# Kernel optimization log

Hardware: AMD Instinct MI355X
Metric: run time of the kernel (lower is better)

The kernel has to match this reference:

```python
import jax, jax.numpy as jnp
import numpy as np

N_TOKENS = 16384
D_MODEL = 1024
N_EXPERTS = 4
TOP_K = 2
LN_EPS = 1e-6


def setup_inputs() -> dict:
    key = jax.random.key(0)
    ks = jax.random.split(key, 6)
    d, e = D_MODEL, N_EXPERTS
    return {
        "x": jax.random.normal(ks[0], (N_TOKENS, d), jnp.float32),
        "gate_w": jax.random.normal(ks[1], (e, d), jnp.float32) * (1.0 / np.sqrt(d)),
        "w1": jax.random.normal(ks[2], (e, 2 * d, d), jnp.float32) * (1.0 / np.sqrt(d)),
        "b1": jax.random.normal(ks[3], (e, 2 * d), jnp.float32) * 0.01,
        "w2": jax.random.normal(ks[4], (e, d, 2 * d), jnp.float32) * (1.0 / np.sqrt(2 * d)),
        "b2": jax.random.normal(ks[5], (e, d), jnp.float32) * 0.01,
        "gamma": jnp.ones((e, d), jnp.float32),
        "beta": jnp.zeros((e, d), jnp.float32),
    }


def _expert_ffn(x, w1e, b1e, w2e, b2e, ge, be):
    h = jax.nn.gelu(x @ w1e.T + b1e, approximate=False)   # [N, 2d]
    z = x + (h @ w2e.T + b2e)                              # residual, [N, d]
    mu = jnp.mean(z, axis=-1, keepdims=True)
    var = jnp.var(z, axis=-1, keepdims=True)
    return (z - mu) * jax.lax.rsqrt(var + LN_EPS) * ge + be


def reference(x, gate_w, w1, b1, w2, b2, gamma, beta):
    n = x.shape[0]
    scores = x @ gate_w.T                                  # [N, E]
    ew, ei = jax.lax.top_k(scores, TOP_K)                  # [N, K]
    ew = jax.nn.softmax(ew, axis=-1)
    # combine weights: dense [N, E] routing matrix (each row has K nonzeros)
    comb = jnp.zeros_like(scores).at[jnp.arange(n)[:, None], ei].add(ew)
    y = jnp.zeros_like(x)
    for e in range(N_EXPERTS):  # small fixed expert count
        y = y + comb[:, e:e + 1] * _expert_ffn(x, w1[e], b1[e], w2[e], b2[e], gamma[e], beta[e])
    return y
```

## Files before the change

kernel.cpp:

```cpp
#include <hip/hip_runtime.h>
#include <hip/hip_bf16.h>
#include <math.h>

#define NT 16384
#define DM 1024
#define NE 4

typedef __attribute__((ext_vector_type(8))) short short8;
typedef __attribute__((ext_vector_type(4))) float f32x4;

#define GLDS(g, l)                                                        \
  __builtin_amdgcn_global_load_lds(                                       \
      (const __attribute__((address_space(1))) void*)(g),                 \
      (__attribute__((address_space(3))) void*)(l), 16, 0, 0)

__device__ __forceinline__ float bf2f(short h) {
    union { unsigned u; float f; } v;
    v.u = ((unsigned)(unsigned short)h) << 16;
    return v.f;
}

__global__ __launch_bounds__(256) void detect_kernel(
    const unsigned int* __restrict__ xw, int* __restrict__ flag)
{
    __shared__ int red[4];
    const int t = threadIdx.x;
    int cnt = 0;
    #pragma unroll 4
    for (int i = 0; i < 64; ++i) {
        unsigned w = xw[t * 64 + i];
        unsigned e0 = (w >> 7) & 0xFFu;
        cnt += (e0 >= 100u && e0 <= 150u) ? 1 : 0;
    }
    #pragma unroll
    for (int o = 32; o > 0; o >>= 1) cnt += __shfl_xor(cnt, o);
    if ((t & 63) == 0) red[t >> 6] = cnt;
    __syncthreads();
    if (t == 0) {
        int tot = red[0] + red[1] + red[2] + red[3];
        *flag = (tot > 8192) ? 1 : 0;
    }
}

__global__ __launch_bounds__(256) void init_kernel(
    int* __restrict__ counts, int* __restrict__ idx)
{
    const int t = blockIdx.x * 256 + threadIdx.x;
    idx[t] = 0;
    if (t < NE) counts[t] = 0;
}

__global__ __launch_bounds__(256) void convert_big_kernel(
    const float* __restrict__ src, short* __restrict__ dst, int n,
    const int* __restrict__ flag)
{
    if (*flag) return;
    const int stride = gridDim.x * blockDim.x;
    const int t0 = blockIdx.x * blockDim.x + threadIdx.x;
    const float4* s = (const float4*)src;
    for (int i = t0; i < n / 4; i += stride) {
        float4 v = s[i];
        __hip_bfloat16 b0 = __float2bfloat16(v.x);
        __hip_bfloat16 b1 = __float2bfloat16(v.y);
        __hip_bfloat16 b2 = __float2bfloat16(v.z);
        __hip_bfloat16 b3 = __float2bfloat16(v.w);
        short4 o;
        o.x = *(short*)&b0; o.y = *(short*)&b1;
        o.z = *(short*)&b2; o.w = *(short*)&b3;
        *(short4*)(dst + (size_t)i * 4) = o;
    }
}

__global__ __launch_bounds__(256) void convert_small_kernel(
    const void* __restrict__ b1, const void* __restrict__ b2,
    const void* __restrict__ ga, const void* __restrict__ be,
    short* __restrict__ b1d, short* __restrict__ b2d,
    short* __restrict__ gad, short* __restrict__ bed,
    const int* __restrict__ flag)
{
    const int isbf = *flag;
    const int t = blockIdx.x * 256 + threadIdx.x;
    const void* src; short* dst; int i;
    if (t < 8192)      { src = b1; dst = b1d; i = t; }
    else if (t < 12288){ src = b2; dst = b2d; i = t - 8192; }
    else if (t < 16384){ src = ga; dst = gad; i = t - 12288; }
    else               { src = be; dst = bed; i = t - 16384; }
    short v;
    if (isbf) v = ((const short*)src)[i];
    else {
        __hip_bfloat16 b = __float2bfloat16(((const float*)src)[i]);
        v = *(short*)&b;
    }
    dst[i] = v;
}

__global__ __launch_bounds__(256) void gate_kernel(
    const void* __restrict__ x, const void* __restrict__ gw,
    float* __restrict__ comb, int* __restrict__ choice,
    const int* __restrict__ flag)
{
    const int lane  = threadIdx.x & 63;
    const int token = blockIdx.x * 4 + (threadIdx.x >> 6);
    double s0 = 0., s1 = 0., s2 = 0., s3 = 0.;
    if (*flag) {
        const short8* xr = (const short8*)((const short*)x + (size_t)token * DM);
        const short8* g0 = (const short8*)((const short*)gw + 0 * DM);
        const short8* g1 = (const short8*)((const short*)gw + 1 * DM);
        const short8* g2 = (const short8*)((const short*)gw + 2 * DM);
        const short8* g3 = (const short8*)((const short*)gw + 3 * DM);
        #pragma unroll
        for (int c = 0; c < 2; ++c) {
            short8 xv = xr[c * 64 + lane];
            short8 a0 = g0[c * 64 + lane], a1 = g1[c * 64 + lane];
            short8 a2 = g2[c * 64 + lane], a3 = g3[c * 64 + lane];
            #pragma unroll
            for (int j = 0; j < 8; ++j) {
                double xd = (double)bf2f(xv[j]);
                s0 += xd * (double)bf2f(a0[j]);
                s1 += xd * (double)bf2f(a1[j]);
                s2 += xd * (double)bf2f(a2[j]);
                s3 += xd * (double)bf2f(a3[j]);
            }
        }
    } else {
        const float4* xr = (const float4*)((const float*)x + (size_t)token * DM);
        const float4* g0 = (const float4*)((const float*)gw + 0 * DM);
        const float4* g1 = (const float4*)((const float*)gw + 1 * DM);
        const float4* g2 = (const float4*)((const float*)gw + 2 * DM);
        const float4* g3 = (const float4*)((const float*)gw + 3 * DM);
        #pragma unroll
        for (int c = 0; c < 4; ++c) {
            float4 xv = xr[c * 64 + lane];
            float4 a0 = g0[c * 64 + lane], a1 = g1[c * 64 + lane];
            float4 a2 = g2[c * 64 + lane], a3 = g3[c * 64 + lane];
            s0 += (double)xv.x * a0.x + (double)xv.y * a0.y + (double)xv.z * a0.z + (double)xv.w * a0.w;
            s1 += (double)xv.x * a1.x + (double)xv.y * a1.y + (double)xv.z * a1.z + (double)xv.w * a1.w;
            s2 += (double)xv.x * a2.x + (double)xv.y * a2.y + (double)xv.z * a2.z + (double)xv.w * a2.w;
            s3 += (double)xv.x * a3.x + (double)xv.y * a3.y + (double)xv.z * a3.z + (double)xv.w * a3.w;
        }
    }
    #pragma unroll
    for (int off = 32; off > 0; off >>= 1) {
        s0 += __shfl_xor(s0, off);
        s1 += __shfl_xor(s1, off);
        s2 += __shfl_xor(s2, off);
        s3 += __shfl_xor(s3, off);
    }
    if (lane == 0) {
        double s[4] = {s0, s1, s2, s3};
        int i1 = 0;
        #pragma unroll
        for (int e = 1; e < 4; ++e) if (s[e] > s[i1]) i1 = e;
        int i2 = -1;
        #pragma unroll
        for (int e = 0; e < 4; ++e) {
            if (e == i1) continue;
            if (i2 < 0 || s[e] > s[i2]) i2 = e;
        }
        float e2 = expf((float)(s[i2] - s[i1]));
        float wa = 1.0f / (1.0f + e2);
        float wb = e2 * wa;
        float* cr = comb + (size_t)token * 4;
        #pragma unroll
        for (int e = 0; e < 4; ++e)
            cr[e] = (e == i1) ? wa : ((e == i2) ? wb : 0.0f);
        choice[token] = i1 | (i2 << 8);
    }
}

__global__ __launch_bounds__(256) void route_kernel(
    const int* __restrict__ choice, int* __restrict__ counts, int* __restrict__ idx)
{
    __shared__ int T[4][8];
    __shared__ int base[4];
    const int tid = threadIdx.x, w = tid >> 6, lane = tid & 63;
    const int t = blockIdx.x * 256 + tid;
    const int c = choice[t];
    const int e0 = c & 0xFF, e1 = (c >> 8) & 0xFF;
    const unsigned long long lt = ((unsigned long long)1 << lane) - 1;
    int rank0 = 0, rank1 = 0;
    #pragma unroll
    for (int e = 0; e < 4; ++e) {
        unsigned long long m0 = __ballot(e0 == e);
        unsigned long long m1 = __ballot(e1 == e);
        if (e0 == e) rank0 = __popcll(m0 & lt);
        if (e1 == e) rank1 = __popcll(m1 & lt);
        if (lane == 0) { T[w][e] = __popcll(m0); T[w][4 + e] = __popcll(m1); }
    }
    __syncthreads();
    if (tid < 4) {
        int tot = 0;
        #pragma unroll
        for (int w2 = 0; w2 < 4; ++w2) tot += T[w2][tid] + T[w2][4 + tid];
        base[tid] = atomicAdd(&counts[tid], tot);
    }
    __syncthreads();
    int off0 = base[e0], off1 = base[e1];
    #pragma unroll
    for (int w2 = 0; w2 < 4; ++w2) {
        if (w2 < w) off0 += T[w2][e0];
        off1 += T[w2][e1];
        if (w2 < w) off1 += T[w2][4 + e1];
    }
    idx[e0 * NT + off0 + rank0] = t;
    idx[e1 * NT + off1 + rank1] = t;
}

template <int EPI>
__global__ __launch_bounds__(256, 2) void gemm_bt(
    const short* __restrict__ Araw, const short* __restrict__ Acvt,
    const short* __restrict__ Braw, const short* __restrict__ Bcvt,
    const __hip_bfloat16* __restrict__ bias,
    void* __restrict__ Cout,
    const int* __restrict__ idxl,
    const int* __restrict__ count, int c0,
    int N, int K, const int* __restrict__ flag)
{
    const int cnt  = *count - c0;
    const int row0 = blockIdx.y * 128;
    if (row0 >= cnt) return;

    const short* A = (*flag) ? Araw : Acvt;
    const short* B = (*flag) ? Braw : Bcvt;

    __shared__ __align__(16) short sA[128 * 64];
    __shared__ __align__(16) short sB[128 * 64];
    const int tid  = threadIdx.x;
    const int wid  = tid >> 6;
    const int lane = tid & 63;
    const int col0 = blockIdx.x * 128;
    const int wm = wid >> 1, wn = wid & 1;
    const int quad = lane >> 4;
    const int mrow = lane & 15;

    const short* gA[4];
    const short* gB[4];
    #pragma unroll
    for (int r = 0; r < 4; ++r) {
        const int lrow = row0 + wid * 32 + r * 8 + (lane >> 3);
        size_t grow;
        if (EPI == 0) {
            int p = c0 + lrow;
            if (p > NT - 1) p = NT - 1;
            grow = (size_t)idxl[p];
        } else {
            grow = (size_t)lrow;
        }
        gA[r] = A + grow * K + (lane & 7) * 8;
        gB[r] = B + (size_t)(col0 + wid * 32 + r * 8 + (lane >> 3)) * K + (lane & 7) * 8;
    }

    f32x4 acc[4][4];
    #pragma unroll
    for (int i = 0; i < 4; ++i)
        #pragma unroll
        for (int j = 0; j < 4; ++j)
            acc[i][j] = (f32x4){0.f, 0.f, 0.f, 0.f};

    for (int k0 = 0; k0 < K; k0 += 64) {
        #pragma unroll
        for (int r = 0; r < 4; ++r) {
            const int rb = wid * 32 + r * 8;
            GLDS(gA[r] + k0, sA + rb * 64);
            GLDS(gB[r] + k0, sB + rb * 64);
        }
        __syncthreads();
        #pragma unroll
        for (int kk = 0; kk < 64; kk += 32) {
            short8 a[4], b[4];
            #pragma unroll
            for (int t = 0; t < 4; ++t) {
                a[t] = *(const short8*)(sA + (wm * 64 + t * 16 + mrow) * 64 + kk + quad * 8);
                b[t] = *(const short8*)(sB + (wn * 64 + t * 16 + mrow) * 64 + kk + quad * 8);
            }
            #pragma unroll
            for (int mt = 0; mt < 4; ++mt)
                #pragma unroll
                for (int nt = 0; nt < 4; ++nt)
                    acc[mt][nt] = __builtin_amdgcn_mfma_f32_16x16x32_bf16(
                        a[mt], b[nt], acc[mt][nt], 0, 0, 0);
        }
        __syncthreads();
    }

    #pragma unroll
    for (int mt = 0; mt < 4; ++mt) {
        #pragma unroll
        for (int nt = 0; nt < 4; ++nt) {
            const int col = col0 + wn * 64 + nt * 16 + mrow;
            const float bval = __bfloat162float(bias[col]);
            #pragma unroll
            for (int i = 0; i < 4; ++i) {
                const int lrow = row0 + wm * 64 + mt * 16 + quad * 4 + i;
                if (lrow < cnt) {
                    float v = acc[mt][nt][i] + bval;
                    if (EPI == 0) {
                        v = 0.5f * v * (1.0f + erff(v * 0.70710678118654752f));
                        ((__hip_bfloat16*)Cout)[(size_t)lrow * N + col] = __float2bfloat16(v);
                    } else {
                        ((float*)Cout)[(size_t)lrow * N + col] = v;
                    }
                }
            }
        }
    }
}

__global__ __launch_bounds__(256) void ln_kernel(
    const float* __restrict__ z,
    const void* __restrict__ xraw,
    const float* __restrict__ comb,
    const int* __restrict__ choice,
    const __hip_bfloat16* __restrict__ gamma,
    const __hip_bfloat16* __restrict__ beta,
    void* __restrict__ y,
    const int* __restrict__ idxl,
    const int* __restrict__ count, int c0,
    int expert, const int* __restrict__ flag)
{
    const int isbf = *flag;
    const int lane = threadIdx.x & 63;
    const int l    = blockIdx.x * 4 + (threadIdx.x >> 6);
    const int cnt  = *count - c0;
    if (l >= cnt) return;
    const int token = idxl[c0 + l];
    const int ch = choice[token];
    const int e0 = ch & 0xFF, e1 = (ch >> 8) & 0xFF;
    const int firstexp = e0 < e1 ? e0 : e1;
    const int accumulate = (expert != firstexp);

    const f32x4* zr = (const f32x4*)(z + (size_t)l * DM);
    f32x4 v[4];
    float sum = 0.f, ssq = 0.f;
    #pragma unroll
    for (int c = 0; c < 4; ++c) {
        f32x4 zv = zr[c * 64 + lane];
        if (isbf) {
            short4 xv = *(const short4*)((const short*)xraw + (size_t)token * DM + c * 256 + lane * 4);
            v[c][0] = zv[0] + bf2f(xv.x);
            v[c][1] = zv[1] + bf2f(xv.y);
            v[c][2] = zv[2] + bf2f(xv.z);
            v[c][3] = zv[3] + bf2f(xv.w);
        } else {
            float4 xv = *(const float4*)((const float*)xraw + (size_t)token * DM + c * 256 + lane * 4);
            v[c][0] = zv[0] + xv.x;
            v[c][1] = zv[1] + xv.y;
            v[c][2] = zv[2] + xv.z;
            v[c][3] = zv[3] + xv.w;
        }
        #pragma unroll
        for (int j = 0; j < 4; ++j) { sum += v[c][j]; ssq += v[c][j] * v[c][j]; }
    }
    #pragma unroll
    for (int off = 32; off > 0; off >>= 1) {
        sum += __shfl_xor(sum, off);
        ssq += __shfl_xor(ssq, off);
    }
    const float mu   = sum * (1.0f / DM);
    const float var  = fmaxf(ssq * (1.0f / DM) - mu * mu, 0.0f);
    const float rstd = rsqrtf(var + 1e-6f);
    const float w    = comb[(size_t)token * 4 + expert];
    #pragma unroll
    for (int c = 0; c < 4; ++c) {
        #pragma unroll
        for (int j = 0; j < 4; ++j) {
            const int id = c * 256 + lane * 4 + j;
            const float g = __bfloat162float(gamma[id]);
            const float b = __bfloat162float(beta[id]);
            float o = w * ((v[c][j] - mu) * rstd * g + b);
            if (isbf) {
                __hip_bfloat16* yr = (__hip_bfloat16*)y + (size_t)token * DM;
                if (accumulate) o += __bfloat162float(yr[id]);
                yr[id] = __float2bfloat16(o);
            } else {
                float* yr = (float*)y + (size_t)token * DM;
                if (accumulate) o += yr[id];
                yr[id] = o;
            }
        }
    }
}

extern "C" void kernel_launch(void* const* d_in, const int* in_sizes, int n_in,
                              void* d_out, int out_size, void* d_ws, size_t ws_size,
                              hipStream_t stream)
{
    char* ws = (char*)d_ws;
    size_t off = 0;
    auto alloc = [&](size_t bytes) -> char* {
        char* p = ws + off;
        off = (off + bytes + 255) & ~(size_t)255;
        return p;
    };
    int*   flag   = (int*)  alloc(256);
    float* comb   = (float*)alloc((size_t)NT * 4 * sizeof(float));
    int*   choice = (int*)  alloc((size_t)NT * sizeof(int));
    int*   counts = (int*)  alloc(NE * sizeof(int));
    int*   idx    = (int*)  alloc((size_t)NE * NT * sizeof(int));
    short* b1b    = (short*)alloc((size_t)NE * 2 * DM * 2);
    short* b2b    = (short*)alloc((size_t)NE * DM * 2);
    short* gb     = (short*)alloc((size_t)NE * DM * 2);
    short* bb     = (short*)alloc((size_t)NE * DM * 2);
    short* w1b    = (short*)alloc((size_t)NE * 2 * DM * DM * 2);
    short* w2b    = (short*)alloc((size_t)NE * 2 * DM * DM * 2);
    short* xb     = (short*)alloc((size_t)NT * DM * 2);
    const size_t fixed = off;

    int cap = NT;
    while (cap > 512 && fixed + (size_t)cap * 8192 > ws_size) cap >>= 1;
    short* h = (short*)alloc((size_t)cap * 2 * DM * 2);
    float* z = (float*)alloc((size_t)cap * DM * sizeof(float));

    detect_kernel<<<1, 256, 0, stream>>>((const unsigned int*)d_in[0], flag);
    init_kernel<<<(NE * NT) / 256, 256, 0, stream>>>(counts, idx);

    convert_big_kernel<<<2048, 256, 0, stream>>>((const float*)d_in[0], xb,
                                                 NT * DM, flag);
    convert_big_kernel<<<2048, 256, 0, stream>>>((const float*)d_in[2], w1b,
                                                 NE * 2 * DM * DM, flag);
    convert_big_kernel<<<2048, 256, 0, stream>>>((const float*)d_in[4], w2b,
                                                 NE * 2 * DM * DM, flag);
    convert_small_kernel<<<80, 256, 0, stream>>>(d_in[3], d_in[5], d_in[6], d_in[7],
                                                 b1b, b2b, gb, bb, flag);

    gate_kernel<<<NT / 4, 256, 0, stream>>>(d_in[0], d_in[1], comb, choice, flag);
    route_kernel<<<NT / 256, 256, 0, stream>>>(choice, counts, idx);

    for (int e = 0; e < NE; ++e) {
        const short* w1r = (const short*)d_in[2] + (size_t)e * 2 * DM * DM;
        const short* w2r = (const short*)d_in[4] + (size_t)e * 2 * DM * DM;
        const short* w1c = w1b + (size_t)e * 2 * DM * DM;
        const short* w2c = w2b + (size_t)e * 2 * DM * DM;
        const __hip_bfloat16* b1e = (const __hip_bfloat16*)(b1b + (size_t)e * 2 * DM);
        const __hip_bfloat16* b2e = (const __hip_bfloat16*)(b2b + (size_t)e * DM);
        const __hip_bfloat16* ge  = (const __hip_bfloat16*)(gb + (size_t)e * DM);
        const __hip_bfloat16* be  = (const __hip_bfloat16*)(bb + (size_t)e * DM);
        const int* idx_e = idx + (size_t)e * NT;
        const int* cnt_e = counts + e;

        for (int c0 = 0; c0 < NT; c0 += cap) {
            dim3 g1(2 * DM / 128, cap / 128);
            gemm_bt<0><<<g1, 256, 0, stream>>>((const short*)d_in[0], xb,
                                               w1r, w1c, b1e, (void*)h,
                                               idx_e, cnt_e, c0, 2 * DM, DM, flag);

            dim3 g2(DM / 128, cap / 128);
            gemm_bt<1><<<g2, 256, 0, stream>>>(h, h, w2r, w2c, b2e, (void*)z,
                                               idx_e, cnt_e, c0, DM, 2 * DM, flag);

            ln_kernel<<<cap / 4, 256, 0, stream>>>(z, d_in[0], comb, choice, ge, be,
                                                   d_out, idx_e, cnt_e, c0, e, flag);
        }
    }
}
```

Baseline: 891.3 us.

## Batch all experts into single 256x256 double-buffered GEMM launches and fuse LN combine

Replaces the 128x128 single-buffered GEMM with a 256x256-tile, 512-thread kernel that double-buffers K tiles in LDS. All four experts are processed in one launch per GEMM using blockIdx.z, with outputs packed contiguously by expert. A single fused LayerNorm kernel then combines both chosen experts per token using a new per-token position array. This removes the per-expert launch sequence and the read-modify-write accumulation of the output, and raises data reuse per tile. In exchange it needs a larger workspace, uses 128 KB of LDS per block, and the 256-row tiles waste more padding at expert boundaries.

```diff
diff --git a/kernel.cpp b/kernel.cpp
--- a/kernel.cpp
+++ b/kernel.cpp
@@ -169,7 +169,8 @@
 }
 
 __global__ __launch_bounds__(256) void route_kernel(
-    const int* __restrict__ choice, int* __restrict__ counts, int* __restrict__ idx)
+    const int* __restrict__ choice, int* __restrict__ counts,
+    int* __restrict__ idx, int* __restrict__ pos)
 {
     __shared__ int T[4][8];
     __shared__ int base[4];
@@ -202,103 +203,122 @@
         off1 += T[w2][e1];
         if (w2 < w) off1 += T[w2][4 + e1];
     }
-    idx[e0 * NT + off0 + rank0] = t;
-    idx[e1 * NT + off1 + rank1] = t;
+    const int p0 = off0 + rank0;
+    const int p1 = off1 + rank1;
+    idx[e0 * NT + p0] = t;
+    idx[e1 * NT + p1] = t;
+    pos[t] = p0 | (p1 << 16);
 }
 
 template <int EPI>
-__global__ __launch_bounds__(256, 2) void gemm_bt(
+__global__ __launch_bounds__(512, 2) void gemm256(
     const short* __restrict__ Araw, const short* __restrict__ Acvt,
     const short* __restrict__ Braw, const short* __restrict__ Bcvt,
-    const __hip_bfloat16* __restrict__ bias,
+    const short* __restrict__ biasAll,
     void* __restrict__ Cout,
-    const int* __restrict__ idxl,
-    const int* __restrict__ count, int c0,
-    int N, int K, const int* __restrict__ flag)
-{
-    const int cnt  = *count - c0;
-    const int row0 = blockIdx.y * 128;
+    const int* __restrict__ idxAll,
+    const int* __restrict__ counts,
+    int c0, int N, int K, const int* __restrict__ flag, int eArg)
+{
+    const int e = (eArg < 0) ? (int)blockIdx.z : eArg;
+    const int cnt = counts[e] - c0;
+    const int row0 = (int)blockIdx.y * 256;
     if (row0 >= cnt) return;
 
+    int rowBase = 0;
+    if (eArg < 0) {
+        #pragma unroll
+        for (int i = 0; i < NE; ++i) rowBase += (i < e) ? counts[i] : 0;
+    }
+
     const short* A = (*flag) ? Araw : Acvt;
-    const short* B = (*flag) ? Braw : Bcvt;
-
-    __shared__ __align__(16) short sA[128 * 64];
-    __shared__ __align__(16) short sB[128 * 64];
+    const short* B = ((*flag) ? Braw : Bcvt) + (size_t)e * 2 * DM * DM;
+    const short* bias = biasAll + (size_t)e * N;
+    const int* idxe = idxAll + (size_t)e * NT + c0;
+
+    __shared__ __align__(16) short sLDS[2][2][256 * 64];
+
     const int tid  = threadIdx.x;
     const int wid  = tid >> 6;
-    const int lane = tid & 63;
-    const int col0 = blockIdx.x * 128;
-    const int wm = wid >> 1, wn = wid & 1;
-    const int quad = lane >> 4;
-    const int mrow = lane & 15;
+    const int col0 = (int)blockIdx.x * 256;
+    const int wm = wid >> 2, wn = wid & 3;
+    const int quad = (tid & 63) >> 4;
+    const int mrow = tid & 15;
 
     const short* gA[4];
     const short* gB[4];
     #pragma unroll
-    for (int r = 0; r < 4; ++r) {
-        const int lrow = row0 + wid * 32 + r * 8 + (lane >> 3);
+    for (int i = 0; i < 4; ++i) {
+        const int lr = i * 64 + (tid >> 3);
         size_t grow;
-        if (EPI == 0) {
-            int p = c0 + lrow;
-            if (p > NT - 1) p = NT - 1;
-            grow = (size_t)idxl[p];
-        } else {
-            grow = (size_t)lrow;
-        }
-        gA[r] = A + grow * K + (lane & 7) * 8;
-        gB[r] = B + (size_t)(col0 + wid * 32 + r * 8 + (lane >> 3)) * K + (lane & 7) * 8;
-    }
-
-    f32x4 acc[4][4];
-    #pragma unroll
-    for (int i = 0; i < 4; ++i)
-        #pragma unroll
-        for (int j = 0; j < 4; ++j)
-            acc[i][j] = (f32x4){0.f, 0.f, 0.f, 0.f};
-
-    for (int k0 = 0; k0 < K; k0 += 64) {
-        #pragma unroll
-        for (int r = 0; r < 4; ++r) {
-            const int rb = wid * 32 + r * 8;
-            GLDS(gA[r] + k0, sA + rb * 64);
-            GLDS(gB[r] + k0, sB + rb * 64);
+        if (EPI == 0) grow = (size_t)idxe[row0 + lr];
+        else          grow = (size_t)(rowBase + row0 + lr);
+        gA[i] = A + grow * (size_t)K + (tid & 7) * 8;
+        gB[i] = B + (size_t)(col0 + lr) * K + (tid & 7) * 8;
+    }
+
+    f32x4 acc[8][4];
+    #pragma unroll
+    for (int m = 0; m < 8; ++m)
+        #pragma unroll
+        for (int n = 0; n < 4; ++n)
+            acc[m][n] = (f32x4){0.f, 0.f, 0.f, 0.f};
+
+    auto stage = [&](int buf, int k0) {
+        short* dA = &sLDS[buf][0][0] + wid * 512;
+        short* dB = &sLDS[buf][1][0] + wid * 512;
+        #pragma unroll
+        for (int i = 0; i < 4; ++i) {
+            GLDS(gA[i] + k0, dA + i * 4096);
+            GLDS(gB[i] + k0, dB + i * 4096);
+        }
+    };
+
+    const int ntiles = K / 64;
+    stage(0, 0);
+    __syncthreads();
+    int cur = 0;
+    for (int t = 0; t < ntiles; ++t) {
+        if (t + 1 < ntiles) stage(cur ^ 1, (t + 1) * 64);
+        const short* sA = &sLDS[cur][0][0];
+        const short* sB = &sLDS[cur][1][0];
+        #pragma unroll
+        for (int kk = 0; kk < 64; kk += 32) {
+            short8 a[8], b[4];
+            #pragma unroll
+            for (int m = 0; m < 8; ++m)
+                a[m] = *(const short8*)(sA + (wm * 128 + m * 16 + mrow) * 64 + kk + quad * 8);
+            #pragma unroll
+            for (int n = 0; n < 4; ++n)
+                b[n] = *(const short8*)(sB + (wn * 64 + n * 16 + mrow) * 64 + kk + quad * 8);
+            #pragma unroll
+            for (int m = 0; m < 8; ++m)
+                #pragma unroll
+                for (int n = 0; n < 4; ++n)
+                    acc[m][n] = __builtin_amdgcn_mfma_f32_16x16x32_bf16(
+                        a[m], b[n], acc[m][n], 0, 0, 0);
         }
         __syncthreads();
-        #pragma unroll
-        for (int kk = 0; kk < 64; kk += 32) {
-            short8 a[4], b[4];
-            #pragma unroll
-            for (int t = 0; t < 4; ++t) {
-                a[t] = *(const short8*)(sA + (wm * 64 + t * 16 + mrow) * 64 + kk + quad * 8);
-                b[t] = *(const short8*)(sB + (wn * 64 + t * 16 + mrow) * 64 + kk + quad * 8);
-            }
-            #pragma unroll
-            for (int mt = 0; mt < 4; ++mt)
-                #pragma unroll
-                for (int nt = 0; nt < 4; ++nt)
-                    acc[mt][nt] = __builtin_amdgcn_mfma_f32_16x16x32_bf16(
-                        a[mt], b[nt], acc[mt][nt], 0, 0, 0);
-        }
-        __syncthreads();
-    }
-
-    #pragma unroll
-    for (int mt = 0; mt < 4; ++mt) {
-        #pragma unroll
-        for (int nt = 0; nt < 4; ++nt) {
-            const int col = col0 + wn * 64 + nt * 16 + mrow;
-            const float bval = __bfloat162float(bias[col]);
+        cur ^= 1;
+    }
+
+    #pragma unroll
+    for (int m = 0; m < 8; ++m) {
+        #pragma unroll
+        for (int n = 0; n < 4; ++n) {
+            const int col = col0 + wn * 64 + n * 16 + mrow;
+            const float bval = bf2f(bias[col]);
             #pragma unroll
             for (int i = 0; i < 4; ++i) {
-                const int lrow = row0 + wm * 64 + mt * 16 + quad * 4 + i;
+                const int lrow = row0 + wm * 128 + m * 16 + quad * 4 + i;
                 if (lrow < cnt) {
-                    float v = acc[mt][nt][i] + bval;
+                    float v = acc[m][n][i] + bval;
                     if (EPI == 0) {
                         v = 0.5f * v * (1.0f + erff(v * 0.70710678118654752f));
-                        ((__hip_bfloat16*)Cout)[(size_t)lrow * N + col] = __float2bfloat16(v);
+                        ((__hip_bfloat16*)Cout)[(size_t)(rowBase + lrow) * N + col] =
+                            __float2bfloat16(v);
                     } else {
-                        ((float*)Cout)[(size_t)lrow * N + col] = v;
+                        ((float*)Cout)[(size_t)(rowBase + lrow) * N + col] = v;
                     }
                 }
             }
@@ -306,15 +326,102 @@
     }
 }
 
-__global__ __launch_bounds__(256) void ln_kernel(
+__global__ __launch_bounds__(256) void ln_fused_kernel(
     const float* __restrict__ z,
     const void* __restrict__ xraw,
     const float* __restrict__ comb,
     const int* __restrict__ choice,
+    const int* __restrict__ pos,
+    const short* __restrict__ gammaAll,
+    const short* __restrict__ betaAll,
+    void* __restrict__ y,
+    const int* __restrict__ counts, const int* __restrict__ flag)
+{
+    const int isbf = *flag;
+    const int lane = threadIdx.x & 63;
+    const int t = blockIdx.x * 4 + (threadIdx.x >> 6);
+
+    const int ca = counts[0], cb = counts[1], cc = counts[2];
+    const int ch = choice[t];
+    const int e0 = ch & 0xFF, e1 = (ch >> 8) & 0xFF;
+    const int pp = pos[t];
+    const int p0 = pp & 0xFFFF, p1 = (pp >> 16) & 0xFFFF;
+    const int b0r = (e0 > 0 ? ca : 0) + (e0 > 1 ? cb : 0) + (e0 > 2 ? cc : 0);
+    const int b1r = (e1 > 0 ? ca : 0) + (e1 > 1 ? cb : 0) + (e1 > 2 ? cc : 0);
+    const float w0 = comb[(size_t)t * 4 + e0];
+    const float w1 = comb[(size_t)t * 4 + e1];
+
+    const f32x4* z0r = (const f32x4*)(z + (size_t)(b0r + p0) * DM);
+    const f32x4* z1r = (const f32x4*)(z + (size_t)(b1r + p1) * DM);
+
+    f32x4 v0[4], v1[4];
+    float s0 = 0.f, q0 = 0.f, s1 = 0.f, q1 = 0.f;
+    #pragma unroll
+    for (int c = 0; c < 4; ++c) {
+        f32x4 a = z0r[c * 64 + lane];
+        f32x4 b = z1r[c * 64 + lane];
+        float xf[4];
+        if (isbf) {
+            short4 xv = *(const short4*)((const short*)xraw + (size_t)t * DM + c * 256 + lane * 4);
+            xf[0] = bf2f(xv.x); xf[1] = bf2f(xv.y); xf[2] = bf2f(xv.z); xf[3] = bf2f(xv.w);
+        } else {
+            float4 xv = *(const float4*)((const float*)xraw + (size_t)t * DM + c * 256 + lane * 4);
+            xf[0] = xv.x; xf[1] = xv.y; xf[2] = xv.z; xf[3] = xv.w;
+        }
+        #pragma unroll
+        for (int j = 0; j < 4; ++j) {
+            v0[c][j] = a[j] + xf[j];
+            v1[c][j] = b[j] + xf[j];
+            s0 += v0[c][j]; q0 += v0[c][j] * v0[c][j];
+            s1 += v1[c][j]; q1 += v1[c][j] * v1[c][j];
+        }
+    }
+    #pragma unroll
+    for (int o = 32; o > 0; o >>= 1) {
+        s0 += __shfl_xor(s0, o); q0 += __shfl_xor(q0, o);
+        s1 += __shfl_xor(s1, o); q1 += __shfl_xor(q1, o);
+    }
+    const float mu0 = s0 * (1.0f / DM);
+    const float r0  = rsqrtf(fmaxf(q0 * (1.0f / DM) - mu0 * mu0, 0.0f) + 1e-6f);
+    const float mu1 = s1 * (1.0f / DM);
+    const float r1  = rsqrtf(fmaxf(q1 * (1.0f / DM) - mu1 * mu1, 0.0f) + 1e-6f);
+
+    #pragma unroll
+    for (int c = 0; c < 4; ++c) {
+        const int id = c * 256 + lane * 4;
+        short4 g0v  = *(const short4*)(gammaAll + (size_t)e0 * DM + id);
+        short4 be0v = *(const short4*)(betaAll  + (size_t)e0 * DM + id);
+        short4 g1v  = *(const short4*)(gammaAll + (size_t)e1 * DM + id);
+        short4 be1v = *(const short4*)(betaAll  + (size_t)e1 * DM + id);
+        const float g0f[4]  = {bf2f(g0v.x),  bf2f(g0v.y),  bf2f(g0v.z),  bf2f(g0v.w)};
+        const float b0f[4]  = {bf2f(be0v.x), bf2f(be0v.y), bf2f(be0v.z), bf2f(be0v.w)};
+        const float g1f[4]  = {bf2f(g1v.x),  bf2f(g1v.y),  bf2f(g1v.z),  bf2f(g1v.w)};
+        const float b1f[4]  = {bf2f(be1v.x), bf2f(be1v.y), bf2f(be1v.z), bf2f(be1v.w)};
+        float o[4];
+        #pragma unroll
+        for (int j = 0; j < 4; ++j)
+            o[j] = w0 * ((v0[c][j] - mu0) * r0 * g0f[j] + b0f[j])
+                 + w1 * ((v1[c][j] - mu1) * r1 * g1f[j] + b1f[j]);
+        if (isbf) {
+            short4 ov;
+            __hip_bfloat16 t0 = __float2bfloat16(o[0]); ov.x = *(short*)&t0;
+            __hip_bfloat16 t1 = __float2bfloat16(o[1]); ov.y = *(short*)&t1;
+            __hip_bfloat16 t2 = __float2bfloat16(o[2]); ov.z = *(short*)&t2;
+            __hip_bfloat16 t3 = __float2bfloat16(o[3]); ov.w = *(short*)&t3;
+            *(short4*)((short*)y + (size_t)t * DM + id) = ov;
+        } else {
+            float4 ov = {o[0], o[1], o[2], o[3]};
+            *(float4*)((float*)y + (size_t)t * DM + id) = ov;
+        }
+    }
+}
+
+__global__ __launch_bounds__(256) void ln_kernel(
+    const float* __restrict__ z, const void* __restrict__ xraw,
+    const float* __restrict__ comb, const int* __restrict__ choice,
     const __hip_bfloat16* __restrict__ gamma,
     const __hip_bfloat16* __restrict__ beta,
-    void* __restrict__ y,
-    const int* __restrict__ idxl,
+    void* __restrict__ y, const int* __restrict__ idxl,
     const int* __restrict__ count, int c0,
     int expert, const int* __restrict__ flag)
 {
@@ -397,6 +504,7 @@
     int*   choice = (int*)  alloc((size_t)NT * sizeof(int));
     int*   counts = (int*)  alloc(NE * sizeof(int));
     int*   idx    = (int*)  alloc((size_t)NE * NT * sizeof(int));
+    int*   pos    = (int*)  alloc((size_t)NT * sizeof(int));
     short* b1b    = (short*)alloc((size_t)NE * 2 * DM * 2);
     short* b2b    = (short*)alloc((size_t)NE * DM * 2);
     short* gb     = (short*)alloc((size_t)NE * DM * 2);
@@ -406,10 +514,9 @@
     short* xb     = (short*)alloc((size_t)NT * DM * 2);
     const size_t fixed = off;
 
-    int cap = NT;
-    while (cap > 512 && fixed + (size_t)cap * 8192 > ws_size) cap >>= 1;
-    short* h = (short*)alloc((size_t)cap * 2 * DM * 2);
-    float* z = (float*)alloc((size_t)cap * DM * sizeof(float));
+    const size_t needH = (size_t)(2 * NT + 256) * (2 * DM) * sizeof(short);
+    const size_t needZ = (size_t)(2 * NT + 256) * DM * sizeof(float);
+    const int batched = (fixed + needH + needZ + 1024) <= ws_size;
 
     detect_kernel<<<1, 256, 0, stream>>>((const unsigned int*)d_in[0], flag);
     init_kernel<<<(NE * NT) / 256, 256, 0, stream>>>(counts, idx);
@@ -424,32 +531,45 @@
                                                  b1b, b2b, gb, bb, flag);
 
     gate_kernel<<<NT / 4, 256, 0, stream>>>(d_in[0], d_in[1], comb, choice, flag);
-    route_kernel<<<NT / 256, 256, 0, stream>>>(choice, counts, idx);
-
-    for (int e = 0; e < NE; ++e) {
-        const short* w1r = (const short*)d_in[2] + (size_t)e * 2 * DM * DM;
-        const short* w2r = (const short*)d_in[4] + (size_t)e * 2 * DM * DM;
-        const short* w1c = w1b + (size_t)e * 2 * DM * DM;
-        const short* w2c = w2b + (size_t)e * 2 * DM * DM;
-        const __hip_bfloat16* b1e = (const __hip_bfloat16*)(b1b + (size_t)e * 2 * DM);
-        const __hip_bfloat16* b2e = (const __hip_bfloat16*)(b2b + (size_t)e * DM);
-        const __hip_bfloat16* ge  = (const __hip_bfloat16*)(gb + (size_t)e * DM);
-        const __hip_bfloat16* be  = (const __hip_bfloat16*)(bb + (size_t)e * DM);
-        const int* idx_e = idx + (size_t)e * NT;
-        const int* cnt_e = counts + e;
-
-        for (int c0 = 0; c0 < NT; c0 += cap) {
-            dim3 g1(2 * DM / 128, cap / 128);
-            gemm_bt<0><<<g1, 256, 0, stream>>>((const short*)d_in[0], xb,
-                                               w1r, w1c, b1e, (void*)h,
-                                               idx_e, cnt_e, c0, 2 * DM, DM, flag);
-
-            dim3 g2(DM / 128, cap / 128);
-            gemm_bt<1><<<g2, 256, 0, stream>>>(h, h, w2r, w2c, b2e, (void*)z,
-                                               idx_e, cnt_e, c0, DM, 2 * DM, flag);
-
-            ln_kernel<<<cap / 4, 256, 0, stream>>>(z, d_in[0], comb, choice, ge, be,
-                                                   d_out, idx_e, cnt_e, c0, e, flag);
-        }
-    }
-}
+    route_kernel<<<NT / 256, 256, 0, stream>>>(choice, counts, idx, pos);
+
+    if (batched) {
+        short* h = (short*)alloc(needH);
+        float* z = (float*)alloc(needZ);
+        dim3 g1(2 * DM / 256, NT / 256, NE);
+        gemm256<0><<<g1, 512, 0, stream>>>((const short*)d_in[0], xb,
+                                           (const short*)d_in[2], w1b, b1b,
+                                           (void*)h, idx, counts, 0,
+                                           2 * DM, DM, flag, -1);
+        dim3 g2(DM / 256, NT / 256, NE);
+        gemm256<1><<<g2, 512, 0, stream>>>(h, h,
+                                           (const short*)d_in[4], w2b, b2b,
+                                           (void*)z, idx, counts, 0,
+                                           DM, 2 * DM, flag, -1);
+        ln_fused_kernel<<<NT / 4, 256, 0, stream>>>(z, d_in[0], comb, choice, pos,
+                                                    gb, bb, d_out, counts, flag);
+    } else {
+        int cap = NT;
+        while (cap > 512 && fixed + (size_t)cap * 8192 > ws_size) cap >>= 1;
+        short* h = (short*)alloc((size_t)cap * 2 * DM * 2);
+        float* z = (float*)alloc((size_t)cap * DM * sizeof(float));
+        for (int e = 0; e < NE; ++e) {
+            for (int c0 = 0; c0 < NT; c0 += cap) {
+                dim3 g1(2 * DM / 256, cap / 256, 1);
+                gemm256<0><<<g1, 512, 0, stream>>>((const short*)d_in[0], xb,
+                                                   (const short*)d_in[2], w1b, b1b,
+                                                   (void*)h, idx, counts, c0,
+                                                   2 * DM, DM, flag, e);
+                dim3 g2(DM / 256, cap / 256, 1);
+                gemm256<1><<<g2, 512, 0, stream>>>(h, h,
+                                                   (const short*)d_in[4], w2b, b2b,
+                                                   (void*)z, idx, counts, c0,
+                                                   DM, 2 * DM, flag, e);
+                ln_kernel<<<cap / 4, 256, 0, stream>>>(z, d_in[0], comb, choice,
+                    (const __hip_bfloat16*)(gb + (size_t)e * DM),
+                    (const __hip_bfloat16*)(bb + (size_t)e * DM),
+                    d_out, idx + (size_t)e * NT, counts + e, c0, e, flag);
+            }
+        }
+    }
+}
```

Measured after the change: 961.5 us. +7.9%, slower.
